# Kernel optimization log

Measured on AMD Instinct MI355X. Metric: run time of the kernel, lower is better.

Reference implementation:

```python
import jax, jax.numpy as jnp
import numpy as np

B, N_NODE, FN, FE = 8, 128, 64, 64  # batch, n_node, n_node_fea, n_edge_fea


def setup_inputs() -> dict:
    key = jax.random.key(0)
    k = jax.random.split(key, 7)
    stdv_w = 1.0 / np.sqrt(2 * FN + FE)  # torch reset uses 1/sqrt(size(0))
    stdv_b = 1.0 / np.sqrt(FN)
    return {
        "H": jax.random.normal(k[0], (B, N_NODE, FN), jnp.float32),
        "A": jax.random.uniform(k[1], (B, N_NODE, N_NODE), jnp.float32),
        "E": jax.random.normal(k[2], (B, N_NODE, N_NODE, FE), jnp.float32),
        "W_att": jax.random.uniform(k[3], (2 * FN + FE, FN), jnp.float32, -stdv_w, stdv_w),
        "W_nei": jax.random.uniform(k[4], (2 * FN + FE, FN), jnp.float32, -stdv_w, stdv_w),
        "bias_att": jax.random.uniform(k[5], (FN,), jnp.float32, -stdv_b, stdv_b),
        "bias_nei": jax.random.uniform(k[6], (FN,), jnp.float32, -stdv_b, stdv_b),
        "N": N_NODE,
    }


def _branch(H, A, E, W, bias, fn):
    # (A[...,None] * cat(H_i, H_j, E)) @ W + bias, computed without
    # materializing the [B,N,N,2F+Fe] concat: split W into row blocks.
    f = H.shape[-1]
    Wi, Wj, We = W[:f], W[f:2 * f], W[2 * f:]
    proj = (
        jnp.einsum('bif,fl->bil', H, Wi)[:, :, None, :]   # H_i broadcast over j
        + jnp.einsum('bjf,fl->bjl', H, Wj)[:, None, :, :] # H_j broadcast over i
        + jnp.einsum('bije,el->bijl', E, We)
    )
    return A[..., None] * proj + bias  # [B, N, N, F]


def reference(H, A, E, W_att, W_nei, bias_att, bias_nei, N):
    att = _branch(H, A, E, W_att, bias_att, None)
    conv = _branch(H, A, E, W_nei, bias_nei, None)
    gated = jax.nn.sigmoid(att) * jax.nn.relu(conv)  # [B, N, N, F]
    return jnp.sum(gated, axis=1)  # sum over first node axis -> [B, N, F]
```

## Files before the change

### kernel.cpp

```cpp
#include <hip/hip_runtime.h>

#define NB 8
#define NNODE 128
#define NF 64

typedef _Float16 half8 __attribute__((ext_vector_type(8)));
typedef float floatx4 __attribute__((ext_vector_type(4)));

#define PSTR (NB * NNODE * NF)

__global__ __launch_bounds__(256)
void proj_kernel(const float* __restrict__ H, const float* __restrict__ Wa,
                 const float* __restrict__ Wn, float* __restrict__ P,
                 float* __restrict__ out_zero) {
  int idx = blockIdx.x * 256 + threadIdx.x;
  int l = idx & 63;
  int node = idx >> 6;
  const float* h = H + node * 64;
  float pia = 0.f, pja = 0.f, pin = 0.f, pjn = 0.f;
#pragma unroll 8
  for (int f = 0; f < 64; ++f) {
    float hv = h[f];
    pia += hv * Wa[f * 64 + l];
    pja += hv * Wa[(64 + f) * 64 + l];
    pin += hv * Wn[f * 64 + l];
    pjn += hv * Wn[(64 + f) * 64 + l];
  }
  int off = node * 64 + l;
  P[off] = pia;
  P[PSTR + off] = pja;
  P[2 * PSTR + off] = pin;
  P[3 * PSTR + off] = pjn;
  out_zero[idx] = 0.f;
}

__global__ __launch_bounds__(256, 2)
void amp_main(const float* __restrict__ A, const float* __restrict__ E,
              const float* __restrict__ Wa, const float* __restrict__ Wn,
              const float* __restrict__ ba, const float* __restrict__ bn,
              const float* __restrict__ P, float* __restrict__ out) {
  const int bx = blockIdx.x;
  const int b = bx >> 6;
  const int rem = bx & 63;
  const int jt = rem >> 3;
  const int ch = rem & 7;
  const int w = threadIdx.x >> 6;
  const int lane = threadIdx.x & 63;
  const int quad = lane >> 4;
  const int l15 = lane & 15;
  const int i0 = ch * 16 + w * 4;
  const int j0 = jt * 16;

  half8 wf[2][4][2];
  const float* Wptr[2] = {Wa, Wn};
#pragma unroll
  for (int br = 0; br < 2; ++br)
#pragma unroll
    for (int t = 0; t < 4; ++t)
#pragma unroll
      for (int hh = 0; hh < 2; ++hh) {
        const float* wsrc = Wptr[br] + (128 + hh * 32 + quad * 8) * 64 + t * 16 + l15;
        half8 v;
#pragma unroll
        for (int x = 0; x < 8; ++x) v[x] = (_Float16)wsrc[x * 64];
        wf[br][t][hh] = v;
      }

  float pj[2][4][4];
#pragma unroll
  for (int br = 0; br < 2; ++br) {
    const float* psrc = P + (br ? 3 * PSTR : PSTR) + (b * 128 + j0) * 64;
#pragma unroll
    for (int t = 0; t < 4; ++t)
#pragma unroll
      for (int r = 0; r < 4; ++r)
        pj[br][t][r] = psrc[(quad * 4 + r) * 64 + t * 16 + l15];
  }
  float biasv[2][4];
#pragma unroll
  for (int t = 0; t < 4; ++t) {
    biasv[0][t] = ba[t * 16 + l15];
    biasv[1][t] = bn[t * 16 + l15];
  }

  float acc[4][4];
#pragma unroll
  for (int t = 0; t < 4; ++t)
#pragma unroll
    for (int r = 0; r < 4; ++r) acc[t][r] = 0.f;

#pragma unroll
  for (int ii = 0; ii < 4; ++ii) {
    const int i = i0 + ii;
    const float* erow = E + ((size_t)((b * 128 + i) * 128 + j0 + l15)) * 64 + quad * 8;
    const float4 e0 = *reinterpret_cast<const float4*>(erow);
    const float4 e1 = *reinterpret_cast<const float4*>(erow + 4);
    const float4 e2 = *reinterpret_cast<const float4*>(erow + 32);
    const float4 e3 = *reinterpret_cast<const float4*>(erow + 36);
    half8 a0, a1;
    a0[0] = (_Float16)e0.x; a0[1] = (_Float16)e0.y; a0[2] = (_Float16)e0.z; a0[3] = (_Float16)e0.w;
    a0[4] = (_Float16)e1.x; a0[5] = (_Float16)e1.y; a0[6] = (_Float16)e1.z; a0[7] = (_Float16)e1.w;
    a1[0] = (_Float16)e2.x; a1[1] = (_Float16)e2.y; a1[2] = (_Float16)e2.z; a1[3] = (_Float16)e2.w;
    a1[4] = (_Float16)e3.x; a1[5] = (_Float16)e3.y; a1[6] = (_Float16)e3.z; a1[7] = (_Float16)e3.w;

    float pia[4], pin[4];
    const float* pisrc = P + (b * 128 + i) * 64;
#pragma unroll
    for (int t = 0; t < 4; ++t) {
      pia[t] = pisrc[t * 16 + l15];
      pin[t] = pisrc[2 * PSTR + t * 16 + l15];
    }
    const float4 av4 = *reinterpret_cast<const float4*>(
        A + (b * 128 + i) * 128 + j0 + quad * 4);
    const float av[4] = {av4.x, av4.y, av4.z, av4.w};

#pragma unroll
    for (int t = 0; t < 4; ++t) {
      floatx4 z = {0.f, 0.f, 0.f, 0.f};
      floatx4 pa = __builtin_amdgcn_mfma_f32_16x16x32_f16(a0, wf[0][t][0], z, 0, 0, 0);
      pa = __builtin_amdgcn_mfma_f32_16x16x32_f16(a1, wf[0][t][1], pa, 0, 0, 0);
      floatx4 pn = __builtin_amdgcn_mfma_f32_16x16x32_f16(a0, wf[1][t][0], z, 0, 0, 0);
      pn = __builtin_amdgcn_mfma_f32_16x16x32_f16(a1, wf[1][t][1], pn, 0, 0, 0);
#pragma unroll
      for (int r = 0; r < 4; ++r) {
        float att = av[r] * (pa[r] + pia[t] + pj[0][t][r]) + biasv[0][t];
        float cnv = av[r] * (pn[r] + pin[t] + pj[1][t][r]) + biasv[1][t];
        float ex = __expf(-att);
        float sig = __builtin_amdgcn_rcpf(1.0f + ex);
        acc[t][r] += sig * fmaxf(cnv, 0.f);
      }
    }
  }

  __shared__ float red[4][16][64];
#pragma unroll
  for (int t = 0; t < 4; ++t)
#pragma unroll
    for (int r = 0; r < 4; ++r)
      red[w][quad * 4 + r][t * 16 + l15] = acc[t][r];
  __syncthreads();

  const int tid = threadIdx.x;
#pragma unroll
  for (int k = 0; k < 4; ++k) {
    int idx = k * 256 + tid;
    int jl = idx >> 6;
    int l = idx & 63;
    float s = red[0][jl][l] + red[1][jl][l] + red[2][jl][l] + red[3][jl][l];
    atomicAdd(out + (b * 128 + j0 + jl) * 64 + l, s);
  }
}

extern "C" void kernel_launch(void* const* d_in, const int* in_sizes, int n_in,
                              void* d_out, int out_size, void* d_ws, size_t ws_size,
                              hipStream_t stream) {
  const float* H = (const float*)d_in[0];
  const float* A = (const float*)d_in[1];
  const float* E = (const float*)d_in[2];
  const float* Wa = (const float*)d_in[3];
  const float* Wn = (const float*)d_in[4];
  const float* ba = (const float*)d_in[5];
  const float* bn = (const float*)d_in[6];
  float* out = (float*)d_out;
  float* P = (float*)d_ws;

  proj_kernel<<<256, 256, 0, stream>>>(H, Wa, Wn, P, out);
  amp_main<<<512, 256, 0, stream>>>(A, E, Wa, Wn, ba, bn, P, out);
}
```

Measured before the change: 99.88 us.

## Fuse node projection into main kernel using MFMA and shuffles

Removes the separate projection kernel and its workspace round trip. Each block now computes the H_i·W_i and H_j·W_j projections for its own tile with fp16 MFMA, and uses lane shuffles to hand each wave its i-row values. The output is zeroed with hipMemsetAsync instead. This trades a launch and global traffic for redundant per-block projection work, extra strided W loads, and lower (fp16) precision on the node projections.

After: 99.34 us. Within noise of the previous version (-0.5%).

```diff
diff --git a/kernel.cpp b/kernel.cpp
--- a/kernel.cpp
+++ b/kernel.cpp
@@ -1,44 +1,22 @@
 #include <hip/hip_runtime.h>
 
-#define NB 8
-#define NNODE 128
-#define NF 64
 
 typedef _Float16 half8 __attribute__((ext_vector_type(8)));
 typedef float floatx4 __attribute__((ext_vector_type(4)));
 
-#define PSTR (NB * NNODE * NF)
-
-__global__ __launch_bounds__(256)
-void proj_kernel(const float* __restrict__ H, const float* __restrict__ Wa,
-                 const float* __restrict__ Wn, float* __restrict__ P,
-                 float* __restrict__ out_zero) {
-  int idx = blockIdx.x * 256 + threadIdx.x;
-  int l = idx & 63;
-  int node = idx >> 6;
-  const float* h = H + node * 64;
-  float pia = 0.f, pja = 0.f, pin = 0.f, pjn = 0.f;
-#pragma unroll 8
-  for (int f = 0; f < 64; ++f) {
-    float hv = h[f];
-    pia += hv * Wa[f * 64 + l];
-    pja += hv * Wa[(64 + f) * 64 + l];
-    pin += hv * Wn[f * 64 + l];
-    pjn += hv * Wn[(64 + f) * 64 + l];
-  }
-  int off = node * 64 + l;
-  P[off] = pia;
-  P[PSTR + off] = pja;
-  P[2 * PSTR + off] = pin;
-  P[3 * PSTR + off] = pjn;
-  out_zero[idx] = 0.f;
+__device__ __forceinline__ half8 cvt2(const float4 a, const float4 b) {
+  half8 v;
+  v[0] = (_Float16)a.x; v[1] = (_Float16)a.y; v[2] = (_Float16)a.z; v[3] = (_Float16)a.w;
+  v[4] = (_Float16)b.x; v[5] = (_Float16)b.y; v[6] = (_Float16)b.z; v[7] = (_Float16)b.w;
+  return v;
 }
 
 __global__ __launch_bounds__(256, 2)
-void amp_main(const float* __restrict__ A, const float* __restrict__ E,
-              const float* __restrict__ Wa, const float* __restrict__ Wn,
-              const float* __restrict__ ba, const float* __restrict__ bn,
-              const float* __restrict__ P, float* __restrict__ out) {
+void amp_fused(const float* __restrict__ H, const float* __restrict__ A,
+               const float* __restrict__ E,
+               const float* __restrict__ Wa, const float* __restrict__ Wn,
+               const float* __restrict__ ba, const float* __restrict__ bn,
+               float* __restrict__ out) {
   const int bx = blockIdx.x;
   const int b = bx >> 6;
   const int rem = bx & 63;
@@ -48,11 +26,51 @@
   const int lane = threadIdx.x & 63;
   const int quad = lane >> 4;
   const int l15 = lane & 15;
-  const int i0 = ch * 16 + w * 4;
+  const int i0b = ch * 16;
+  const int i0 = i0b + w * 4;
   const int j0 = jt * 16;
+  const float* Wptr[2] = {Wa, Wn};
+
+  half8 hi[2], hj[2];
+  {
+    const float* hib = H + (b * 128 + i0b + l15) * 64 + quad * 8;
+    const float* hjb = H + (b * 128 + j0 + l15) * 64 + quad * 8;
+#pragma unroll
+    for (int hh = 0; hh < 2; ++hh) {
+      hi[hh] = cvt2(*reinterpret_cast<const float4*>(hib + hh * 32),
+                    *reinterpret_cast<const float4*>(hib + hh * 32 + 4));
+      hj[hh] = cvt2(*reinterpret_cast<const float4*>(hjb + hh * 32),
+                    *reinterpret_cast<const float4*>(hjb + hh * 32 + 4));
+    }
+  }
+
+  float pia_all[2][4][4];
+  float pj[2][4][4];
+  for (int br = 0; br < 2; ++br) {
+    const float* W = Wptr[br];
+#pragma unroll
+    for (int t = 0; t < 4; ++t) {
+      floatx4 z = {0.f, 0.f, 0.f, 0.f};
+      floatx4 pif = z, pjf = z;
+#pragma unroll
+      for (int hh = 0; hh < 2; ++hh) {
+        const float* wi = W + (hh * 32 + quad * 8) * 64 + t * 16 + l15;
+        const float* wj = W + (64 + hh * 32 + quad * 8) * 64 + t * 16 + l15;
+        half8 bi, bj;
+#pragma unroll
+        for (int x = 0; x < 8; ++x) { bi[x] = (_Float16)wi[x * 64]; bj[x] = (_Float16)wj[x * 64]; }
+        pif = __builtin_amdgcn_mfma_f32_16x16x32_f16(hi[hh], bi, pif, 0, 0, 0);
+        pjf = __builtin_amdgcn_mfma_f32_16x16x32_f16(hj[hh], bj, pjf, 0, 0, 0);
+      }
+#pragma unroll
+      for (int r = 0; r < 4; ++r) pj[br][t][r] = pjf[r];
+#pragma unroll
+      for (int ii = 0; ii < 4; ++ii)
+        pia_all[br][t][ii] = __shfl(pif[ii], w * 16 + l15);
+    }
+  }
 
   half8 wf[2][4][2];
-  const float* Wptr[2] = {Wa, Wn};
 #pragma unroll
   for (int br = 0; br < 2; ++br)
 #pragma unroll
@@ -66,16 +84,6 @@
         wf[br][t][hh] = v;
       }
 
-  float pj[2][4][4];
-#pragma unroll
-  for (int br = 0; br < 2; ++br) {
-    const float* psrc = P + (br ? 3 * PSTR : PSTR) + (b * 128 + j0) * 64;
-#pragma unroll
-    for (int t = 0; t < 4; ++t)
-#pragma unroll
-      for (int r = 0; r < 4; ++r)
-        pj[br][t][r] = psrc[(quad * 4 + r) * 64 + t * 16 + l15];
-  }
   float biasv[2][4];
 #pragma unroll
   for (int t = 0; t < 4; ++t) {
@@ -93,23 +101,11 @@
   for (int ii = 0; ii < 4; ++ii) {
     const int i = i0 + ii;
     const float* erow = E + ((size_t)((b * 128 + i) * 128 + j0 + l15)) * 64 + quad * 8;
-    const float4 e0 = *reinterpret_cast<const float4*>(erow);
-    const float4 e1 = *reinterpret_cast<const float4*>(erow + 4);
-    const float4 e2 = *reinterpret_cast<const float4*>(erow + 32);
-    const float4 e3 = *reinterpret_cast<const float4*>(erow + 36);
-    half8 a0, a1;
-    a0[0] = (_Float16)e0.x; a0[1] = (_Float16)e0.y; a0[2] = (_Float16)e0.z; a0[3] = (_Float16)e0.w;
-    a0[4] = (_Float16)e1.x; a0[5] = (_Float16)e1.y; a0[6] = (_Float16)e1.z; a0[7] = (_Float16)e1.w;
-    a1[0] = (_Float16)e2.x; a1[1] = (_Float16)e2.y; a1[2] = (_Float16)e2.z; a1[3] = (_Float16)e2.w;
-    a1[4] = (_Float16)e3.x; a1[5] = (_Float16)e3.y; a1[6] = (_Float16)e3.z; a1[7] = (_Float16)e3.w;
+    half8 a0 = cvt2(*reinterpret_cast<const float4*>(erow),
+                    *reinterpret_cast<const float4*>(erow + 4));
+    half8 a1 = cvt2(*reinterpret_cast<const float4*>(erow + 32),
+                    *reinterpret_cast<const float4*>(erow + 36));
 
-    float pia[4], pin[4];
-    const float* pisrc = P + (b * 128 + i) * 64;
-#pragma unroll
-    for (int t = 0; t < 4; ++t) {
-      pia[t] = pisrc[t * 16 + l15];
-      pin[t] = pisrc[2 * PSTR + t * 16 + l15];
-    }
     const float4 av4 = *reinterpret_cast<const float4*>(
         A + (b * 128 + i) * 128 + j0 + quad * 4);
     const float av[4] = {av4.x, av4.y, av4.z, av4.w};
@@ -123,8 +119,8 @@
       pn = __builtin_amdgcn_mfma_f32_16x16x32_f16(a1, wf[1][t][1], pn, 0, 0, 0);
 #pragma unroll
       for (int r = 0; r < 4; ++r) {
-        float att = av[r] * (pa[r] + pia[t] + pj[0][t][r]) + biasv[0][t];
-        float cnv = av[r] * (pn[r] + pin[t] + pj[1][t][r]) + biasv[1][t];
+        float att = av[r] * (pa[r] + pia_all[0][t][ii] + pj[0][t][r]) + biasv[0][t];
+        float cnv = av[r] * (pn[r] + pia_all[1][t][ii] + pj[1][t][r]) + biasv[1][t];
         float ex = __expf(-att);
         float sig = __builtin_amdgcn_rcpf(1.0f + ex);
         acc[t][r] += sig * fmaxf(cnv, 0.f);
@@ -162,8 +158,7 @@
   const float* ba = (const float*)d_in[5];
   const float* bn = (const float*)d_in[6];
   float* out = (float*)d_out;
-  float* P = (float*)d_ws;
 
-  proj_kernel<<<256, 256, 0, stream>>>(H, Wa, Wn, P, out);
-  amp_main<<<512, 256, 0, stream>>>(A, E, Wa, Wn, ba, bn, P, out);
+  hipMemsetAsync(d_out, 0, (size_t)out_size * sizeof(float), stream);
+  amp_fused<<<512, 256, 0, stream>>>(H, A, E, Wa, Wn, ba, bn, out);
 }
```
